# Performance work log

Hardware: AMD Instinct MI355X
Metric: run time of the kernel (lower is better)

Reference implementation:

```python
import jax, jax.numpy as jnp
import numpy as np

EPS = 1e-5


def setup_inputs() -> dict:
    key = jax.random.key(0)
    ks = jax.random.split(key, 4)
    N, E, D, L = 100000, 1600000, 128, 3
    x = jax.random.normal(ks[0], (N, D), dtype=jnp.float32)
    edge_index = jax.random.randint(ks[1], (2, E), 0, N, dtype=jnp.int64)
    # torch Linear weight layout [out, in]; kaiming-ish scale
    W = jax.random.normal(ks[2], (L, D, D), dtype=jnp.float32) / np.sqrt(D)
    b = jnp.zeros((L, D), dtype=jnp.float32)
    gamma = jnp.ones((L, D), dtype=jnp.float32)
    beta = jnp.zeros((L, D), dtype=jnp.float32)
    return {"x": x, "edge_index": edge_index, "W": W, "b": b,
            "gamma": gamma, "beta": beta}


def reference(x, edge_index, W, b, gamma, beta):
    N = x.shape[0]
    L = W.shape[0]
    # add_self_loops
    loops = jnp.arange(N, dtype=edge_index.dtype)
    ei = jnp.concatenate([edge_index, jnp.stack([loops, loops])], axis=1)
    row, col = ei[0], ei[1]  # source, target (PyG source_to_target flow)
    # degree of target nodes (includes self loops)
    deg = jax.ops.segment_sum(jnp.ones(col.shape, x.dtype), col, num_segments=N)
    deg_inv_sqrt = jnp.where(deg > 0, deg ** -0.5, jnp.array(0.0, x.dtype))
    norm = deg_inv_sqrt[row] * deg_inv_sqrt[col]  # [E+N]
    for l in range(L):
        h = x @ W[l].T  # Linear, no bias
        # gather source messages, scale, scatter-add to targets
        out = jax.ops.segment_sum(norm[:, None] * h[row], col, num_segments=N)
        out = out + b[l]
        # NodeNorm 'm': subtract per-node (row) mean over features
        out = out - jnp.mean(out, axis=1, keepdims=True)
        # BatchNorm1d (training mode: biased batch stats over node axis)
        mu = jnp.mean(out, axis=0)
        var = jnp.var(out, axis=0)
        x = gamma[l] * (out - mu) * jax.lax.rsqrt(var + EPS) + beta[l]
    return x
```

## Files before the change

### kernel.cpp

```cpp
#include <hip/hip_runtime.h>

#define D 128
#define EPSV 1e-5f

typedef _Float16 f16;
typedef __attribute__((ext_vector_type(8))) _Float16 f16x8;
typedef __attribute__((ext_vector_type(4))) _Float16 f16x4;
typedef __attribute__((ext_vector_type(4))) float f32x4;

__global__ void fold_kernel(const float* __restrict__ W, const float* __restrict__ scsh,
                            int use_id, f16* __restrict__ Wfo, float* __restrict__ shW) {
    const int o = blockIdx.x;
    const int k = threadIdx.x;
    float w = W[o * D + k];
    float sc = use_id ? 1.0f : scsh[k];
    float sh = use_id ? 0.0f : scsh[D + k];
    Wfo[o * D + k] = (f16)(w * sc);
    float v = sh * w;
    #pragma unroll
    for (int off = 1; off < 64; off <<= 1) v += __shfl_xor(v, off, 64);
    __shared__ float red[2];
    if ((k & 63) == 0) red[k >> 6] = v;
    __syncthreads();
    if (k == 0) shW[o] = red[0] + red[1];
}

__global__ __launch_bounds__(256) void bcount_kernel(const int* __restrict__ col,
                                                     int* __restrict__ gb, int E, int seg) {
    __shared__ int s[4096];
    for (int j = threadIdx.x; j < seg; j += 256) s[j] = 0;
    __syncthreads();
    int i = blockIdx.x * 256 + threadIdx.x;
    const int stride = gridDim.x * 256;
    for (; i < E; i += stride) {
        int b = col[i] >> 8;
        int p = (i >> 8) & 7;
        atomicAdd(&s[b * 8 + p], 1);
    }
    __syncthreads();
    for (int j = threadIdx.x; j < seg; j += 256)
        if (s[j]) atomicAdd(&gb[j], s[j]);
}

__global__ __launch_bounds__(1024) void bscan_kernel(const int* __restrict__ gb,
                                                     int* __restrict__ soff,
                                                     int* __restrict__ cur) {
    __shared__ int s[1024];
    const int tid = threadIdx.x;
    const int base = tid * 4;
    int g0 = gb[base], g1 = gb[base + 1], g2 = gb[base + 2], g3 = gb[base + 3];
    int my = g0 + g1 + g2 + g3;
    s[tid] = my;
    __syncthreads();
    for (int off = 1; off < 1024; off <<= 1) {
        int t = (tid >= off) ? s[tid - off] : 0;
        __syncthreads();
        s[tid] += t;
        __syncthreads();
    }
    int ex = s[tid] - my;
    soff[base] = ex;           cur[(base + 0) * 16] = ex;  ex += g0;
    soff[base + 1] = ex;       cur[(base + 1) * 16] = ex;  ex += g1;
    soff[base + 2] = ex;       cur[(base + 2) * 16] = ex;  ex += g2;
    soff[base + 3] = ex;       cur[(base + 3) * 16] = ex;
    if (tid == 1023) soff[4096] = s[1023];
}

__global__ __launch_bounds__(256) void bfill_kernel(const int* __restrict__ row,
                                                    const int* __restrict__ col,
                                                    int* __restrict__ cur,
                                                    int2* __restrict__ bpairs, int E) {
    int i = blockIdx.x * 256 + threadIdx.x;
    const int stride = gridDim.x * 256;
    for (; i < E; i += stride) {
        int c = col[i];
        int b = c >> 8;
        int p = (i >> 8) & 7;
        int pos = atomicAdd(&cur[(b * 8 + p) * 16], 1);
        bpairs[pos] = make_int2(row[i], c);
    }
}

__global__ __launch_bounds__(256) void bdeg_kernel(const int2* __restrict__ bpairs,
                                                   const int* __restrict__ soff,
                                                   int* __restrict__ deg,
                                                   float* __restrict__ dis, int N) {
    __shared__ int dc[256];
    const int b = blockIdx.x;
    const int tid = threadIdx.x;
    dc[tid] = 0;
    __syncthreads();
    const int s0 = soff[b * 8], s1 = soff[(b + 1) * 8];
    for (int k = s0 + tid; k < s1; k += 256)
        atomicAdd(&dc[bpairs[k].y & 255], 1);
    __syncthreads();
    int c = (b << 8) + tid;
    if (c < N) {
        int dv = dc[tid];
        deg[c] = dv;
        dis[c] = rsqrtf((float)dv + 1.0f);
    }
}

__global__ void scan1_kernel(const int* __restrict__ cnt, int* __restrict__ offs,
                             int* __restrict__ bsum, int N) {
    __shared__ int s[256];
    int tid = threadIdx.x;
    int i = blockIdx.x * 256 + tid;
    int v = (i < N) ? cnt[i] : 0;
    s[tid] = v;
    __syncthreads();
    for (int off = 1; off < 256; off <<= 1) {
        int t = (tid >= off) ? s[tid - off] : 0;
        __syncthreads();
        s[tid] += t;
        __syncthreads();
    }
    if (i < N) offs[i] = s[tid] - v;
    if (tid == 255) bsum[blockIdx.x] = s[255];
}

__global__ void scan2_kernel(int* __restrict__ bsum, int NB) {
    __shared__ int s[512];
    int tid = threadIdx.x;
    int v = (tid < NB) ? bsum[tid] : 0;
    s[tid] = v;
    __syncthreads();
    for (int off = 1; off < 512; off <<= 1) {
        int t = (tid >= off) ? s[tid - off] : 0;
        __syncthreads();
        s[tid] += t;
        __syncthreads();
    }
    if (tid < NB) bsum[tid] = s[tid] - v;
}

__global__ void scan3_kernel(int* __restrict__ offs, const int* __restrict__ bsum,
                             int N, int E) {
    int i = blockIdx.x * 256 + threadIdx.x;
    if (i < N) offs[i] += bsum[blockIdx.x];
    if (i == 0) offs[N] = E;
}

__global__ __launch_bounds__(256) void cfill_kernel(const int2* __restrict__ bpairs,
                                                    const int* __restrict__ soff,
                                                    const int* __restrict__ offs,
                                                    int* __restrict__ srcs, int N) {
    __shared__ int lc[256];
    const int b = blockIdx.x;
    const int tid = threadIdx.x;
    int c = (b << 8) + tid;
    lc[tid] = (c < N) ? offs[c] : 0;
    __syncthreads();
    const int s0 = soff[b * 8], s1 = soff[(b + 1) * 8];
    for (int k = s0 + tid; k < s1; k += 256) {
        int2 pr = bpairs[k];
        int pos = atomicAdd(&lc[pr.y & 255], 1);
        srcs[pos] = pr.x;
    }
}

__global__ __launch_bounds__(256) void tsort_kernel(const int* __restrict__ deg,
                                                    int* __restrict__ order, int N) {
    __shared__ int hist[256];
    __shared__ int cur[256];
    __shared__ int cur2[256];
    const int tid = threadIdx.x;
    const int i = blockIdx.x * 256 + tid;
    hist[tid] = 0;
    __syncthreads();
    int b = 0;
    if (i < N) {
        b = 255 - min(deg[i], 255);
        atomicAdd(&hist[b], 1);
    }
    __syncthreads();
    int v = hist[tid];
    cur[tid] = v;
    __syncthreads();
    for (int off = 1; off < 256; off <<= 1) {
        int t = (tid >= off) ? cur[tid - off] : 0;
        __syncthreads();
        cur[tid] += t;
        __syncthreads();
    }
    cur2[tid] = cur[tid] - v;
    __syncthreads();
    if (i < N) {
        int pos = atomicAdd(&cur2[b], 1);
        order[blockIdx.x * 256 + pos] = i;
    }
}


__global__ __launch_bounds__(256) void gemm_kernel(
    const f16* __restrict__ xh, const float* __restrict__ xf32,
    const f16* __restrict__ Wfo, const float* __restrict__ shW,
    const float* __restrict__ dis, f16* __restrict__ h, int N, int nrg)
{
    const int lane = threadIdx.x & 63;
    const int l15 = lane & 15;
    const int lh = lane >> 4;

    f16x8 af[8][4];
    #pragma unroll
    for (int t = 0; t < 8; t++)
        #pragma unroll
        for (int kb = 0; kb < 4; kb++)
            af[t][kb] = *reinterpret_cast<const f16x8*>(
                &Wfo[(t * 16 + l15) * D + kb * 32 + lh * 8]);

    const int wid = (blockIdx.x * blockDim.x + threadIdx.x) >> 6;
    const int nwaves = (gridDim.x * blockDim.x) >> 6;

    for (int rg = wid; rg < nrg; rg += nwaves) {
        int row = rg * 16 + l15;
        int rrow = min(row, N - 1);
        f16x8 bf[4];
        if (xf32) {
            #pragma unroll
            for (int kb = 0; kb < 4; kb++) {
                const float* p = &xf32[(long long)rrow * D + kb * 32 + lh * 8];
                float4 u0 = *reinterpret_cast<const float4*>(p);
                float4 u1 = *reinterpret_cast<const float4*>(p + 4);
                f16x8 b;
                b[0] = (f16)u0.x; b[1] = (f16)u0.y; b[2] = (f16)u0.z; b[3] = (f16)u0.w;
                b[4] = (f16)u1.x; b[5] = (f16)u1.y; b[6] = (f16)u1.z; b[7] = (f16)u1.w;
                bf[kb] = b;
            }
        } else {
            #pragma unroll
            for (int kb = 0; kb < 4; kb++)
                bf[kb] = *reinterpret_cast<const f16x8*>(
                    &xh[(long long)rrow * D + kb * 32 + lh * 8]);
        }
        float d = dis[rrow];
        bool ok = (row < N);

        #pragma unroll
        for (int t = 0; t < 8; t++) {
            f32x4 acc = {0.0f, 0.0f, 0.0f, 0.0f};
            #pragma unroll
            for (int kb = 0; kb < 4; kb++)
                acc = __builtin_amdgcn_mfma_f32_16x16x32_f16(af[t][kb], bf[kb], acc, 0, 0, 0);
            int o0 = t * 16 + lh * 4;
            float4 sw = *reinterpret_cast<const float4*>(&shW[o0]);
            f16x4 ov;
            ov[0] = (f16)(d * (acc[0] + sw.x));
            ov[1] = (f16)(d * (acc[1] + sw.y));
            ov[2] = (f16)(d * (acc[2] + sw.z));
            ov[3] = (f16)(d * (acc[3] + sw.w));
            if (ok)
                *reinterpret_cast<f16x4*>(&h[(long long)row * D + o0]) = ov;
        }
    }
}

__global__ __launch_bounds__(256) void gather_kernel(
    const f16* __restrict__ h, const int* __restrict__ offs,
    const int* __restrict__ srcs, const int* __restrict__ order,
    const float* __restrict__ dis, const float* __restrict__ bias,
    f16* __restrict__ t, float* __restrict__ stats, int N)
{
    const int tid = threadIdx.x;
    const int l16 = tid & 15;
    const int grp = tid >> 4;
    const int f8 = l16 * 8;
    float bv[8];
    {
        float4 ba = *reinterpret_cast<const float4*>(&bias[f8]);
        float4 bb = *reinterpret_cast<const float4*>(&bias[f8 + 4]);
        bv[0] = ba.x; bv[1] = ba.y; bv[2] = ba.z; bv[3] = ba.w;
        bv[4] = bb.x; bv[5] = bb.y; bv[6] = bb.z; bv[7] = bb.w;
    }
    float ssum[8] = {0, 0, 0, 0, 0, 0, 0, 0}, ssq[8] = {0, 0, 0, 0, 0, 0, 0, 0};

    for (int ci = blockIdx.x * 16 + grp; ci < N; ci += gridDim.x * 16) {
        const int c = order[ci];
        f16x8 hv = *reinterpret_cast<const f16x8*>(&h[(long long)c * D + f8]);
        float a[8], a2[8];
        #pragma unroll
        for (int m = 0; m < 8; m++) { a[m] = (float)hv[m]; a2[m] = 0.0f; }
        const int k0 = offs[c], k1 = offs[c + 1];
        for (int kb = k0; kb < k1; kb += 16) {
            int kk = kb + l16;
            int rl = (kk < k1) ? srcs[kk] : 0;
            int cnt = min(16, k1 - kb);
            int j = 0;
            for (; j + 4 <= cnt; j += 4) {
                int r0 = __shfl(rl, j, 16);
                int r1 = __shfl(rl, j + 1, 16);
                int r2 = __shfl(rl, j + 2, 16);
                int r3 = __shfl(rl, j + 3, 16);
                f16x8 v0 = *reinterpret_cast<const f16x8*>(&h[(long long)r0 * D + f8]);
                f16x8 v1 = *reinterpret_cast<const f16x8*>(&h[(long long)r1 * D + f8]);
                f16x8 v2 = *reinterpret_cast<const f16x8*>(&h[(long long)r2 * D + f8]);
                f16x8 v3 = *reinterpret_cast<const f16x8*>(&h[(long long)r3 * D + f8]);
                #pragma unroll
                for (int m = 0; m < 8; m++) {
                    a[m] += (float)v0[m] + (float)v2[m];
                    a2[m] += (float)v1[m] + (float)v3[m];
                }
            }
            for (; j < cnt; j++) {
                int r0 = __shfl(rl, j, 16);
                f16x8 v0 = *reinterpret_cast<const f16x8*>(&h[(long long)r0 * D + f8]);
                #pragma unroll
                for (int m = 0; m < 8; m++) a[m] += (float)v0[m];
            }
        }
        float d = dis[c];
        float tv[8];
        float s = 0.0f;
        #pragma unroll
        for (int m = 0; m < 8; m++) {
            tv[m] = d * (a[m] + a2[m]) + bv[m];
            s += tv[m];
        }
        #pragma unroll
        for (int off = 1; off < 16; off <<= 1) s += __shfl_xor(s, off, 16);
        float mean = s * (1.0f / 128.0f);
        f16x8 ov;
        #pragma unroll
        for (int m = 0; m < 8; m++) {
            tv[m] -= mean;
            ov[m] = (f16)tv[m];
            ssum[m] += tv[m];
            ssq[m] += tv[m] * tv[m];
        }
        *reinterpret_cast<f16x8*>(&t[(long long)c * D + f8]) = ov;
    }

    __shared__ float red[256 * 16];
    #pragma unroll
    for (int j = 0; j < 8; j++) {
        red[tid * 16 + j] = ssum[j];
        red[tid * 16 + 8 + j] = ssq[j];
    }
    __syncthreads();
    const int o = tid;
    const int f = o & 127;
    const int sq = o >> 7;
    const int lf = f >> 3;
    const int j = f & 7;
    float v = 0;
    #pragma unroll
    for (int g = 0; g < 16; g++)
        v += red[(g * 16 + lf) * 16 + sq * 8 + j];
    unsafeAtomicAdd(&stats[o], v);
}

__global__ void stats_kernel(const float* __restrict__ stats,
                             const float* __restrict__ gamma,
                             const float* __restrict__ beta,
                             float* __restrict__ scsh, float Ninv)
{
    int j = threadIdx.x;
    float mu = stats[j] * Ninv;
    float var = stats[D + j] * Ninv - mu * mu;
    float inv = rsqrtf(var + EPSV);
    float sc = gamma[j] * inv;
    scsh[j] = sc;
    scsh[D + j] = beta[j] - mu * sc;
}

__global__ __launch_bounds__(256) void epi2_kernel(
    const f16* __restrict__ t, const float* __restrict__ scsh,
    float* __restrict__ out, long long total4)
{
    __shared__ float sc[D], sh[D];
    if (threadIdx.x < D) {
        sc[threadIdx.x] = scsh[threadIdx.x];
        sh[threadIdx.x] = scsh[D + threadIdx.x];
    }
    __syncthreads();
    long long i = (long long)blockIdx.x * blockDim.x + threadIdx.x;
    const long long stride = (long long)gridDim.x * blockDim.x;
    for (; i < total4; i += stride) {
        f16x4 v = reinterpret_cast<const f16x4*>(t)[i];
        int f0 = (int)((i * 4) & (D - 1));
        float4 o;
        o.x = (float)v[0] * sc[f0 + 0] + sh[f0 + 0];
        o.y = (float)v[1] * sc[f0 + 1] + sh[f0 + 1];
        o.z = (float)v[2] * sc[f0 + 2] + sh[f0 + 2];
        o.w = (float)v[3] * sc[f0 + 3] + sh[f0 + 3];
        reinterpret_cast<float4*>(out)[i] = o;
    }
}

extern "C" void kernel_launch(void* const* d_in, const int* in_sizes, int n_in,
                              void* d_out, int out_size, void* d_ws, size_t ws_size,
                              hipStream_t stream)
{
    const float* x_in  = (const float*)d_in[0];
    const int*   ei    = (const int*)d_in[1];
    const float* W     = (const float*)d_in[2];
    const float* bias  = (const float*)d_in[3];
    const float* gamma = (const float*)d_in[4];
    const float* beta  = (const float*)d_in[5];

    const int N = in_sizes[0] / D;
    const int E = in_sizes[1] / 2;
    const int L = in_sizes[2] / (D * D);
    const int* row = ei;
    const int* col = ei + E;
    const int NB = (N + 255) / 256;
    const int NBUCK = (N + 255) >> 8;
    const int seg = NBUCK * 8;
    const int nrg = (N + 15) / 16;

    f16* tbuf = (f16*)d_ws;
    f16* hbuf = tbuf + (size_t)N * D;
    f16* Wfo  = hbuf + (size_t)N * D;
    float* dis   = (float*)(Wfo + D * D);
    float* stats = dis + N;
    float* scsh  = stats + 2 * D;
    float* shW   = scsh + 2 * D;
    int* deg   = (int*)(shW + D);
    int* offs  = deg + N;
    int* srcs  = offs + (N + 1);
    int* bsum  = srcs + E;
    int* gb    = bsum + 512;
    int* soff  = gb + 4096;
    int* cur   = soff + 4097;
    int* order = cur + 4096 * 16;
    size_t used = (size_t)(order + N - (int*)d_ws);
    int2* bpairs = (int2*)((int*)d_ws + ((used + 1) & ~(size_t)1));

    hipMemsetAsync(gb, 0, 4096 * sizeof(int), stream);
    bcount_kernel<<<128, 256, 0, stream>>>(col, gb, E, seg);
    bscan_kernel<<<1, 1024, 0, stream>>>(gb, soff, cur);
    bfill_kernel<<<1024, 256, 0, stream>>>(row, col, cur, bpairs, E);
    bdeg_kernel<<<NBUCK, 256, 0, stream>>>(bpairs, soff, deg, dis, N);
    scan1_kernel<<<NB, 256, 0, stream>>>(deg, offs, bsum, N);
    scan2_kernel<<<1, 512, 0, stream>>>(bsum, NB);
    scan3_kernel<<<NB, 256, 0, stream>>>(offs, bsum, N, E);
    cfill_kernel<<<NBUCK, 256, 0, stream>>>(bpairs, soff, offs, srcs, N);
    tsort_kernel<<<NB, 256, 0, stream>>>(deg, order, N);

    const float Ninv = 1.0f / (float)N;
    const long long total4 = (long long)N * D / 4;

    fold_kernel<<<D, D, 0, stream>>>(W, scsh, 1, Wfo, shW);

    for (int l = 0; l < L; l++) {
        gemm_kernel<<<512, 256, 0, stream>>>(
            tbuf, (l == 0) ? x_in : nullptr, Wfo, shW, dis, hbuf, N, nrg);
        hipMemsetAsync(stats, 0, 2 * D * sizeof(float), stream);
        gather_kernel<<<2048, 256, 0, stream>>>(
            hbuf, offs, srcs, order, dis, bias + (size_t)l * D, tbuf, stats, N);
        stats_kernel<<<1, D, 0, stream>>>(
            stats, gamma + (size_t)l * D, beta + (size_t)l * D, scsh, Ninv);
        if (l < L - 1)
            fold_kernel<<<D, D, 0, stream>>>(W + (size_t)(l + 1) * D * D, scsh, 0, Wfo, shW);
        else
            epi2_kernel<<<4096, 256, 0, stream>>>(tbuf, scsh, (float*)d_out, total4);
    }
}
```

Before: 484.4 us.

## Pack per-node gather metadata and process two nodes per lane group

```diff
diff --git a/kernel.cpp b/kernel.cpp
--- a/kernel.cpp
+++ b/kernel.cpp
@@ -161,7 +161,9 @@
 }
 
 __global__ __launch_bounds__(256) void tsort_kernel(const int* __restrict__ deg,
-                                                    int* __restrict__ order, int N) {
+                                                    const int* __restrict__ offs,
+                                                    const float* __restrict__ dis,
+                                                    int4* __restrict__ nodeinfo, int N) {
     __shared__ int hist[256];
     __shared__ int cur[256];
     __shared__ int cur2[256];
@@ -169,9 +171,10 @@
     const int i = blockIdx.x * 256 + tid;
     hist[tid] = 0;
     __syncthreads();
-    int b = 0;
+    int b = 0, dv = 0;
     if (i < N) {
-        b = 255 - min(deg[i], 255);
+        dv = deg[i];
+        b = 255 - min(dv, 255);
         atomicAdd(&hist[b], 1);
     }
     __syncthreads();
@@ -188,7 +191,8 @@
     __syncthreads();
     if (i < N) {
         int pos = atomicAdd(&cur2[b], 1);
-        order[blockIdx.x * 256 + pos] = i;
+        nodeinfo[blockIdx.x * 256 + pos] =
+            make_int4(i, offs[i], dv, __float_as_int(dis[i]));
     }
 }
 
@@ -257,10 +261,9 @@
 }
 
 __global__ __launch_bounds__(256) void gather_kernel(
-    const f16* __restrict__ h, const int* __restrict__ offs,
-    const int* __restrict__ srcs, const int* __restrict__ order,
-    const float* __restrict__ dis, const float* __restrict__ bias,
-    f16* __restrict__ t, float* __restrict__ stats, int N)
+    const f16* __restrict__ h, const int4* __restrict__ nodeinfo,
+    const int* __restrict__ srcs, const float* __restrict__ bias,
+    f16* __restrict__ t, float* __restrict__ stats, int N, int E)
 {
     const int tid = threadIdx.x;
     const int l16 = tid & 15;
@@ -275,60 +278,101 @@
     }
     float ssum[8] = {0, 0, 0, 0, 0, 0, 0, 0}, ssq[8] = {0, 0, 0, 0, 0, 0, 0, 0};
 
-    for (int ci = blockIdx.x * 16 + grp; ci < N; ci += gridDim.x * 16) {
-        const int c = order[ci];
-        f16x8 hv = *reinterpret_cast<const f16x8*>(&h[(long long)c * D + f8]);
-        float a[8], a2[8];
+    int ci = blockIdx.x * 32 + grp * 2;
+    const int cstride = gridDim.x * 32;
+    const int4 zero4 = make_int4(0, 0, 0, 0);
+    int4 niA = (ci < N) ? nodeinfo[ci] : zero4;
+    int4 niB = (ci + 1 < N) ? nodeinfo[ci + 1] : zero4;
+
+    for (; ci < N; ci += cstride) {
+        const int cin = ci + cstride;
+        int4 niA_n = (cin < N) ? nodeinfo[cin] : zero4;
+        int4 niB_n = (cin + 1 < N) ? nodeinfo[cin + 1] : zero4;
+
+        const bool v1 = (ci + 1 < N);
+        const int c0 = niA.x, k00 = niA.y, d0 = niA.z;
+        const float dis0 = __int_as_float(niA.w);
+        const int c1 = v1 ? niB.x : c0;
+        const int k10 = v1 ? niB.y : 0;
+        const int d1 = v1 ? niB.z : 0;
+        const float dis1 = v1 ? __int_as_float(niB.w) : 0.0f;
+
+        f16x8 s0v = *reinterpret_cast<const f16x8*>(&h[(long long)c0 * D + f8]);
+        f16x8 s1v = *reinterpret_cast<const f16x8*>(&h[(long long)c1 * D + f8]);
+        float a0[8], a1[8];
         #pragma unroll
-        for (int m = 0; m < 8; m++) { a[m] = (float)hv[m]; a2[m] = 0.0f; }
-        const int k0 = offs[c], k1 = offs[c + 1];
-        for (int kb = k0; kb < k1; kb += 16) {
-            int kk = kb + l16;
-            int rl = (kk < k1) ? srcs[kk] : 0;
-            int cnt = min(16, k1 - kb);
-            int j = 0;
-            for (; j + 4 <= cnt; j += 4) {
-                int r0 = __shfl(rl, j, 16);
-                int r1 = __shfl(rl, j + 1, 16);
-                int r2 = __shfl(rl, j + 2, 16);
-                int r3 = __shfl(rl, j + 3, 16);
-                f16x8 v0 = *reinterpret_cast<const f16x8*>(&h[(long long)r0 * D + f8]);
-                f16x8 v1 = *reinterpret_cast<const f16x8*>(&h[(long long)r1 * D + f8]);
-                f16x8 v2 = *reinterpret_cast<const f16x8*>(&h[(long long)r2 * D + f8]);
-                f16x8 v3 = *reinterpret_cast<const f16x8*>(&h[(long long)r3 * D + f8]);
+        for (int m = 0; m < 8; m++) { a0[m] = (float)s0v[m]; a1[m] = (float)s1v[m]; }
+
+        const int maxd = max(d0, d1);
+        for (int kb = 0; kb < maxd; kb += 16) {
+            int i0 = min(k00 + kb + l16, E - 1);
+            int i1 = min(k10 + kb + l16, E - 1);
+            int rl0 = srcs[i0];
+            int rl1 = srcs[i1];
+            int cnt0 = min(16, d0 - kb);
+            int cnt1 = min(16, d1 - kb);
+            int cmax = max(cnt0, cnt1);
+            for (int j = 0; j < cmax; j += 2) {
+                int r00 = __shfl(rl0, j, 16);
+                int r01 = __shfl(rl0, j + 1, 16);
+                int r10 = __shfl(rl1, j, 16);
+                int r11 = __shfl(rl1, j + 1, 16);
+                float w00 = (j < cnt0) ? 1.0f : 0.0f;
+                float w01 = (j + 1 < cnt0) ? 1.0f : 0.0f;
+                float w10 = (j < cnt1) ? 1.0f : 0.0f;
+                float w11 = (j + 1 < cnt1) ? 1.0f : 0.0f;
+                f16x8 v00 = *reinterpret_cast<const f16x8*>(&h[(long long)r00 * D + f8]);
+                f16x8 v01 = *reinterpret_cast<const f16x8*>(&h[(long long)r01 * D + f8]);
+                f16x8 v10 = *reinterpret_cast<const f16x8*>(&h[(long long)r10 * D + f8]);
+                f16x8 v11 = *reinterpret_cast<const f16x8*>(&h[(long long)r11 * D + f8]);
                 #pragma unroll
                 for (int m = 0; m < 8; m++) {
-                    a[m] += (float)v0[m] + (float)v2[m];
-                    a2[m] += (float)v1[m] + (float)v3[m];
+                    a0[m] = fmaf(w00, (float)v00[m], a0[m]);
+                    a0[m] = fmaf(w01, (float)v01[m], a0[m]);
+                    a1[m] = fmaf(w10, (float)v10[m], a1[m]);
+                    a1[m] = fmaf(w11, (float)v11[m], a1[m]);
                 }
             }
-            for (; j < cnt; j++) {
-                int r0 = __shfl(rl, j, 16);
-                f16x8 v0 = *reinterpret_cast<const f16x8*>(&h[(long long)r0 * D + f8]);
-                #pragma unroll
-                for (int m = 0; m < 8; m++) a[m] += (float)v0[m];
+        }
+
+        {
+            float tv[8], s = 0.0f;
+            #pragma unroll
+            for (int m = 0; m < 8; m++) { tv[m] = dis0 * a0[m] + bv[m]; s += tv[m]; }
+            #pragma unroll
+            for (int off = 1; off < 16; off <<= 1) s += __shfl_xor(s, off, 16);
+            float mean = s * (1.0f / 128.0f);
+            f16x8 ov;
+            #pragma unroll
+            for (int m = 0; m < 8; m++) {
+                tv[m] -= mean;
+                ov[m] = (f16)tv[m];
+                ssum[m] += tv[m];
+                ssq[m] += tv[m] * tv[m];
             }
+            *reinterpret_cast<f16x8*>(&t[(long long)c0 * D + f8]) = ov;
         }
-        float d = dis[c];
-        float tv[8];
-        float s = 0.0f;
-        #pragma unroll
-        for (int m = 0; m < 8; m++) {
-            tv[m] = d * (a[m] + a2[m]) + bv[m];
-            s += tv[m];
+        {
+            float g = v1 ? 1.0f : 0.0f;
+            float tv[8], s = 0.0f;
+            #pragma unroll
+            for (int m = 0; m < 8; m++) { tv[m] = dis1 * a1[m] + bv[m]; s += tv[m]; }
+            #pragma unroll
+            for (int off = 1; off < 16; off <<= 1) s += __shfl_xor(s, off, 16);
+            float mean = s * (1.0f / 128.0f);
+            f16x8 ov;
+            #pragma unroll
+            for (int m = 0; m < 8; m++) {
+                tv[m] -= mean;
+                ov[m] = (f16)tv[m];
+                ssum[m] += g * tv[m];
+                ssq[m] += g * tv[m] * tv[m];
+            }
+            if (v1)
+                *reinterpret_cast<f16x8*>(&t[(long long)c1 * D + f8]) = ov;
         }
-        #pragma unroll
-        for (int off = 1; off < 16; off <<= 1) s += __shfl_xor(s, off, 16);
-        float mean = s * (1.0f / 128.0f);
-        f16x8 ov;
-        #pragma unroll
-        for (int m = 0; m < 8; m++) {
-            tv[m] -= mean;
-            ov[m] = (f16)tv[m];
-            ssum[m] += tv[m];
-            ssq[m] += tv[m] * tv[m];
-        }
-        *reinterpret_cast<f16x8*>(&t[(long long)c * D + f8]) = ov;
+        niA = niA_n;
+        niB = niB_n;
     }
 
     __shared__ float red[256 * 16];
@@ -416,15 +460,17 @@
     float* stats = dis + N;
     float* scsh  = stats + 2 * D;
     float* shW   = scsh + 2 * D;
-    int* deg   = (int*)(shW + D);
+    size_t off16 = (size_t)(shW + D - (float*)d_ws);
+    off16 = (off16 + 3) & ~(size_t)3;
+    int4* nodeinfo = (int4*)((float*)d_ws + off16);
+    int* deg   = (int*)(nodeinfo + NB * 256);
     int* offs  = deg + N;
     int* srcs  = offs + (N + 1);
-    int* bsum  = srcs + E;
+    int* bsum  = srcs + (E + 16);
     int* gb    = bsum + 512;
     int* soff  = gb + 4096;
     int* cur   = soff + 4097;
-    int* order = cur + 4096 * 16;
-    size_t used = (size_t)(order + N - (int*)d_ws);
+    size_t used = (size_t)(cur + 4096 * 16 - (int*)d_ws);
     int2* bpairs = (int2*)((int*)d_ws + ((used + 1) & ~(size_t)1));
 
     hipMemsetAsync(gb, 0, 4096 * sizeof(int), stream);
@@ -436,10 +482,11 @@
     scan2_kernel<<<1, 512, 0, stream>>>(bsum, NB);
     scan3_kernel<<<NB, 256, 0, stream>>>(offs, bsum, N, E);
     cfill_kernel<<<NBUCK, 256, 0, stream>>>(bpairs, soff, offs, srcs, N);
-    tsort_kernel<<<NB, 256, 0, stream>>>(deg, order, N);
+    tsort_kernel<<<NB, 256, 0, stream>>>(deg, offs, dis, nodeinfo, N);
 
     const float Ninv = 1.0f / (float)N;
     const long long total4 = (long long)N * D / 4;
+    const int gblocks = (N + 63) / 64;
 
     fold_kernel<<<D, D, 0, stream>>>(W, scsh, 1, Wfo, shW);
 
@@ -447,8 +494,8 @@
         gemm_kernel<<<512, 256, 0, stream>>>(
             tbuf, (l == 0) ? x_in : nullptr, Wfo, shW, dis, hbuf, N, nrg);
         hipMemsetAsync(stats, 0, 2 * D * sizeof(float), stream);
-        gather_kernel<<<2048, 256, 0, stream>>>(
-            hbuf, offs, srcs, order, dis, bias + (size_t)l * D, tbuf, stats, N);
+        gather_kernel<<<gblocks, 256, 0, stream>>>(
+            hbuf, nodeinfo, srcs, bias + (size_t)l * D, tbuf, stats, N, E);
         stats_kernel<<<1, D, 0, stream>>>(
             stats, gamma + (size_t)l * D, beta + (size_t)l * D, scsh, Ninv);
         if (l < L - 1)
```

Measured after the change: 488.4 us. No clear change (+0.8%).

## Split feature gather into eight column slices for cache locality

Applied to the files above, without the earlier changes.

```diff
diff --git a/kernel.cpp b/kernel.cpp
--- a/kernel.cpp
+++ b/kernel.cpp
@@ -2,6 +2,7 @@
 
 #define D 128
 #define EPSV 1e-5f
+#define NSLICE 8
 
 typedef _Float16 f16;
 typedef __attribute__((ext_vector_type(8))) _Float16 f16x8;
@@ -69,7 +70,7 @@
 __global__ __launch_bounds__(256) void bfill_kernel(const int* __restrict__ row,
                                                     const int* __restrict__ col,
                                                     int* __restrict__ cur,
-                                                    int2* __restrict__ bpairs, int E) {
+                                                    int* __restrict__ bpairs, int E) {
     int i = blockIdx.x * 256 + threadIdx.x;
     const int stride = gridDim.x * 256;
     for (; i < E; i += stride) {
@@ -77,11 +78,11 @@
         int b = c >> 8;
         int p = (i >> 8) & 7;
         int pos = atomicAdd(&cur[(b * 8 + p) * 16], 1);
-        bpairs[pos] = make_int2(row[i], c);
-    }
-}
-
-__global__ __launch_bounds__(256) void bdeg_kernel(const int2* __restrict__ bpairs,
+        bpairs[pos] = (int)(((unsigned)(c & 255) << 24) | (unsigned)row[i]);
+    }
+}
+
+__global__ __launch_bounds__(256) void bdeg_kernel(const int* __restrict__ bpairs,
                                                    const int* __restrict__ soff,
                                                    int* __restrict__ deg,
                                                    float* __restrict__ dis, int N) {
@@ -92,7 +93,7 @@
     __syncthreads();
     const int s0 = soff[b * 8], s1 = soff[(b + 1) * 8];
     for (int k = s0 + tid; k < s1; k += 256)
-        atomicAdd(&dc[bpairs[k].y & 255], 1);
+        atomicAdd(&dc[(unsigned)bpairs[k] >> 24], 1);
     __syncthreads();
     int c = (b << 8) + tid;
     if (c < N) {
@@ -142,7 +143,7 @@
     if (i == 0) offs[N] = E;
 }
 
-__global__ __launch_bounds__(256) void cfill_kernel(const int2* __restrict__ bpairs,
+__global__ __launch_bounds__(256) void cfill_kernel(const int* __restrict__ bpairs,
                                                     const int* __restrict__ soff,
                                                     const int* __restrict__ offs,
                                                     int* __restrict__ srcs, int N) {
@@ -154,14 +155,16 @@
     __syncthreads();
     const int s0 = soff[b * 8], s1 = soff[(b + 1) * 8];
     for (int k = s0 + tid; k < s1; k += 256) {
-        int2 pr = bpairs[k];
-        int pos = atomicAdd(&lc[pr.y & 255], 1);
-        srcs[pos] = pr.x;
+        int pk = bpairs[k];
+        int pos = atomicAdd(&lc[(unsigned)pk >> 24], 1);
+        srcs[pos] = pk & 0x00FFFFFF;
     }
 }
 
 __global__ __launch_bounds__(256) void tsort_kernel(const int* __restrict__ deg,
-                                                    int* __restrict__ order, int N) {
+                                                    const int* __restrict__ offs,
+                                                    const float* __restrict__ dis,
+                                                    int4* __restrict__ nodeinfo, int N) {
     __shared__ int hist[256];
     __shared__ int cur[256];
     __shared__ int cur2[256];
@@ -169,9 +172,10 @@
     const int i = blockIdx.x * 256 + tid;
     hist[tid] = 0;
     __syncthreads();
-    int b = 0;
+    int b = 0, dv = 0;
     if (i < N) {
-        b = 255 - min(deg[i], 255);
+        dv = deg[i];
+        b = 255 - min(dv, 255);
         atomicAdd(&hist[b], 1);
     }
     __syncthreads();
@@ -188,7 +192,8 @@
     __syncthreads();
     if (i < N) {
         int pos = atomicAdd(&cur2[b], 1);
-        order[blockIdx.x * 256 + pos] = i;
+        nodeinfo[blockIdx.x * 256 + pos] =
+            make_int4(i, offs[i], dv, __float_as_int(dis[i]));
     }
 }
 
@@ -251,21 +256,76 @@
             ov[2] = (f16)(d * (acc[2] + sw.z));
             ov[3] = (f16)(d * (acc[3] + sw.w));
             if (ok)
-                *reinterpret_cast<f16x4*>(&h[(long long)row * D + o0]) = ov;
+                *reinterpret_cast<f16x4*>(
+                    &h[((size_t)t * N + row) * 16 + lh * 4]) = ov;
         }
     }
 }
 
-__global__ __launch_bounds__(256) void gather_kernel(
-    const f16* __restrict__ h, const int* __restrict__ offs,
-    const int* __restrict__ srcs, const int* __restrict__ order,
-    const float* __restrict__ dis, const float* __restrict__ bias,
+__global__ __launch_bounds__(256) void gather_slice_kernel(
+    const f16* __restrict__ ht, const int4* __restrict__ nodeinfo,
+    const int* __restrict__ srcs, f16* __restrict__ tp, int N)
+{
+    const int s = blockIdx.x & 7;
+    const int chunk = blockIdx.x >> 3;
+    const int nchunks = gridDim.x >> 3;
+    const int tid = threadIdx.x;
+    const int j = tid & 1;
+    const int grp = tid >> 1;
+    const f16* __restrict__ hs = ht + (size_t)s * N * 16;
+    f16* __restrict__ ts = tp + (size_t)s * N * 16;
+
+    for (int ci = chunk * 128 + grp; ci < N; ci += nchunks * 128) {
+        int4 ni = nodeinfo[ci];
+        const int c = ni.x, k0 = ni.y, deg = ni.z;
+        const float dis = __int_as_float(ni.w);
+
+        f16x8 sv = *reinterpret_cast<const f16x8*>(&hs[(size_t)c * 16 + j * 8]);
+        float a[8];
+        #pragma unroll
+        for (int m = 0; m < 8; m++) a[m] = (float)sv[m];
+
+        int kb = 0;
+        for (; kb + 4 <= deg; kb += 4) {
+            int rl0 = srcs[k0 + kb + j];
+            int rl1 = srcs[k0 + kb + 2 + j];
+            int r0 = __shfl(rl0, 0, 2);
+            int r1 = __shfl(rl0, 1, 2);
+            int r2 = __shfl(rl1, 0, 2);
+            int r3 = __shfl(rl1, 1, 2);
+            f16x8 v0 = *reinterpret_cast<const f16x8*>(&hs[(size_t)r0 * 16 + j * 8]);
+            f16x8 v1 = *reinterpret_cast<const f16x8*>(&hs[(size_t)r1 * 16 + j * 8]);
+            f16x8 v2 = *reinterpret_cast<const f16x8*>(&hs[(size_t)r2 * 16 + j * 8]);
+            f16x8 v3 = *reinterpret_cast<const f16x8*>(&hs[(size_t)r3 * 16 + j * 8]);
+            #pragma unroll
+            for (int m = 0; m < 8; m++)
+                a[m] += ((float)v0[m] + (float)v1[m]) + ((float)v2[m] + (float)v3[m]);
+        }
+        for (; kb < deg; kb++) {
+            int r = srcs[k0 + kb];
+            f16x8 v = *reinterpret_cast<const f16x8*>(&hs[(size_t)r * 16 + j * 8]);
+            #pragma unroll
+            for (int m = 0; m < 8; m++) a[m] += (float)v[m];
+        }
+
+        f16x8 ov;
+        #pragma unroll
+        for (int m = 0; m < 8; m++) ov[m] = (f16)(dis * a[m]);
+        *reinterpret_cast<f16x8*>(&ts[(size_t)c * 16 + j * 8]) = ov;
+    }
+}
+
+__global__ __launch_bounds__(256) void epi1_kernel(
+    const f16* __restrict__ tp, const float* __restrict__ bias,
     f16* __restrict__ t, float* __restrict__ stats, int N)
 {
     const int tid = threadIdx.x;
     const int l16 = tid & 15;
     const int grp = tid >> 4;
     const int f8 = l16 * 8;
+    const int s = f8 >> 4;
+    const int off = f8 & 15;
+    const f16* __restrict__ tps = tp + (size_t)s * N * 16;
     float bv[8];
     {
         float4 ba = *reinterpret_cast<const float4*>(&bias[f8]);
@@ -275,51 +335,14 @@
     }
     float ssum[8] = {0, 0, 0, 0, 0, 0, 0, 0}, ssq[8] = {0, 0, 0, 0, 0, 0, 0, 0};
 
-    for (int ci = blockIdx.x * 16 + grp; ci < N; ci += gridDim.x * 16) {
-        const int c = order[ci];
-        f16x8 hv = *reinterpret_cast<const f16x8*>(&h[(long long)c * D + f8]);
-        float a[8], a2[8];
-        #pragma unroll
-        for (int m = 0; m < 8; m++) { a[m] = (float)hv[m]; a2[m] = 0.0f; }
-        const int k0 = offs[c], k1 = offs[c + 1];
-        for (int kb = k0; kb < k1; kb += 16) {
-            int kk = kb + l16;
-            int rl = (kk < k1) ? srcs[kk] : 0;
-            int cnt = min(16, k1 - kb);
-            int j = 0;
-            for (; j + 4 <= cnt; j += 4) {
-                int r0 = __shfl(rl, j, 16);
-                int r1 = __shfl(rl, j + 1, 16);
-                int r2 = __shfl(rl, j + 2, 16);
-                int r3 = __shfl(rl, j + 3, 16);
-                f16x8 v0 = *reinterpret_cast<const f16x8*>(&h[(long long)r0 * D + f8]);
-                f16x8 v1 = *reinterpret_cast<const f16x8*>(&h[(long long)r1 * D + f8]);
-                f16x8 v2 = *reinterpret_cast<const f16x8*>(&h[(long long)r2 * D + f8]);
-                f16x8 v3 = *reinterpret_cast<const f16x8*>(&h[(long long)r3 * D + f8]);
-                #pragma unroll
-                for (int m = 0; m < 8; m++) {
-                    a[m] += (float)v0[m] + (float)v2[m];
-                    a2[m] += (float)v1[m] + (float)v3[m];
-                }
-            }
-            for (; j < cnt; j++) {
-                int r0 = __shfl(rl, j, 16);
-                f16x8 v0 = *reinterpret_cast<const f16x8*>(&h[(long long)r0 * D + f8]);
-                #pragma unroll
-                for (int m = 0; m < 8; m++) a[m] += (float)v0[m];
-            }
-        }
-        float d = dis[c];
-        float tv[8];
-        float s = 0.0f;
-        #pragma unroll
-        for (int m = 0; m < 8; m++) {
-            tv[m] = d * (a[m] + a2[m]) + bv[m];
-            s += tv[m];
-        }
-        #pragma unroll
-        for (int off = 1; off < 16; off <<= 1) s += __shfl_xor(s, off, 16);
-        float mean = s * (1.0f / 128.0f);
+    for (int c = blockIdx.x * 16 + grp; c < N; c += gridDim.x * 16) {
+        f16x8 v = *reinterpret_cast<const f16x8*>(&tps[(size_t)c * 16 + off]);
+        float tv[8], sum = 0.0f;
+        #pragma unroll
+        for (int m = 0; m < 8; m++) { tv[m] = (float)v[m] + bv[m]; sum += tv[m]; }
+        #pragma unroll
+        for (int o = 1; o < 16; o <<= 1) sum += __shfl_xor(sum, o, 16);
+        float mean = sum * (1.0f / 128.0f);
         f16x8 ov;
         #pragma unroll
         for (int m = 0; m < 8; m++) {
@@ -328,7 +351,7 @@
             ssum[m] += tv[m];
             ssq[m] += tv[m] * tv[m];
         }
-        *reinterpret_cast<f16x8*>(&t[(long long)c * D + f8]) = ov;
+        *reinterpret_cast<f16x8*>(&t[(size_t)c * D + f8]) = ov;
     }
 
     __shared__ float red[256 * 16];
@@ -411,21 +434,23 @@
 
     f16* tbuf = (f16*)d_ws;
     f16* hbuf = tbuf + (size_t)N * D;
-    f16* Wfo  = hbuf + (size_t)N * D;
+    f16* tp   = hbuf + (size_t)N * D;
+    f16* Wfo  = tp + (size_t)N * D;
     float* dis   = (float*)(Wfo + D * D);
     float* stats = dis + N;
     float* scsh  = stats + 2 * D;
     float* shW   = scsh + 2 * D;
-    int* deg   = (int*)(shW + D);
-    int* offs  = deg + N;
-    int* srcs  = offs + (N + 1);
-    int* bsum  = srcs + E;
-    int* gb    = bsum + 512;
-    int* soff  = gb + 4096;
-    int* cur   = soff + 4097;
-    int* order = cur + 4096 * 16;
-    size_t used = (size_t)(order + N - (int*)d_ws);
-    int2* bpairs = (int2*)((int*)d_ws + ((used + 1) & ~(size_t)1));
+    size_t offf = (size_t)(shW + D - (float*)d_ws);
+    offf = (offf + 3) & ~(size_t)3;
+    int4* nodeinfo = (int4*)((float*)d_ws + offf);
+    int* deg    = (int*)(nodeinfo + (size_t)NB * 256);
+    int* offs   = deg + N;
+    int* srcs   = offs + (N + 1);
+    int* bsum   = srcs + (E + 16);
+    int* gb     = bsum + 512;
+    int* soff   = gb + 4096;
+    int* cur    = soff + 4097;
+    int* bpairs = cur + 4096 * 16;
 
     hipMemsetAsync(gb, 0, 4096 * sizeof(int), stream);
     bcount_kernel<<<128, 256, 0, stream>>>(col, gb, E, seg);
@@ -436,7 +461,7 @@
     scan2_kernel<<<1, 512, 0, stream>>>(bsum, NB);
     scan3_kernel<<<NB, 256, 0, stream>>>(offs, bsum, N, E);
     cfill_kernel<<<NBUCK, 256, 0, stream>>>(bpairs, soff, offs, srcs, N);
-    tsort_kernel<<<NB, 256, 0, stream>>>(deg, order, N);
+    tsort_kernel<<<NB, 256, 0, stream>>>(deg, offs, dis, nodeinfo, N);
 
     const float Ninv = 1.0f / (float)N;
     const long long total4 = (long long)N * D / 4;
@@ -446,9 +471,9 @@
     for (int l = 0; l < L; l++) {
         gemm_kernel<<<512, 256, 0, stream>>>(
             tbuf, (l == 0) ? x_in : nullptr, Wfo, shW, dis, hbuf, N, nrg);
+        gather_slice_kernel<<<2048, 256, 0, stream>>>(hbuf, nodeinfo, srcs, tp, N);
         hipMemsetAsync(stats, 0, 2 * D * sizeof(float), stream);
-        gather_kernel<<<2048, 256, 0, stream>>>(
-            hbuf, offs, srcs, order, dis, bias + (size_t)l * D, tbuf, stats, N);
+        epi1_kernel<<<2048, 256, 0, stream>>>(tp, bias + (size_t)l * D, tbuf, stats, N);
         stats_kernel<<<1, D, 0, stream>>>(
             stats, gamma + (size_t)l * D, beta + (size_t)l * D, scsh, Ninv);
         if (l < L - 1)
```

Measured after the change: 768.7 us. +58.7%, slower.
